# Kernel optimization log

Measured on AMD Instinct MI355X. Metric: run time of the kernel, lower is better.

Reference implementation:

```python
import jax, jax.numpy as jnp
import numpy as np

B = 2; D = 256; NH = 8; NL = 4; HD = D // NH
K = 2; P = K * K; NV = 4; DFF = 1024
SHAPES = ((128, 128), (64, 64), (32, 32), (16, 16))
LV = sum(h * w for h, w in SHAPES)
START = np.cumsum([0] + [h * w for h, w in SHAPES])[:-1].tolist()
EPS = 1e-5

# fixed 2x2 sampling kernel, matching _create_kernel_indices (even kernel branch)
_ind = np.linspace(-0.5, 0.5, K)
_ii, _jj = np.meshgrid(_ind, _ind, indexing='ij')
KERNEL = jnp.asarray(np.stack([_jj, _ii], -1).reshape(-1, 2) / K, jnp.float32)  # (P,2)


def _layer_norm(x, w, b):
    m = x.mean(-1, keepdims=True)
    v = ((x - m) ** 2).mean(-1, keepdims=True)
    return (x - m) * jax.lax.rsqrt(v + EPS) * w + b


def _box_attention(query, value, ref_windows, vpw, vpb, opw, opb, boxw, boxb, attw, attb):
    b, lq, _ = query.shape
    # value projection, split into heads: (b, NH, LV, HD)
    v = (value @ vpw.T + vpb).reshape(b, LV, NH, HD).transpose(0, 2, 1, 3)

    # attention weights: softmax over all (level, point) jointly per head
    aw = query @ attw.T + attb
    aw = jax.nn.softmax(aw.reshape(b, lq, NH, NL * P), -1).reshape(b, lq, NH, NL, P)

    # where to attend (with_rotation=False -> 4 offset variables, angle from ref)
    ob = (query @ boxw.T + boxb).reshape(b, lq, NH, NL, NV)
    rw = ref_windows[:, :, None, None, :]                    # (b,lq,1,1,7)
    ref_boxes = rw[..., jnp.array([0, 1, 3, 4])]
    angles = jnp.broadcast_to(rw[..., 6:7], (b, lq, NH, NL, 1))
    boxes = ref_boxes + ob / 8.0 * ref_boxes[..., jnp.array([2, 3, 2, 3])]
    center = boxes[..., None, :2]                            # (b,lq,NH,NL,1,2)
    size = boxes[..., None, 2:]
    c, s = jnp.cos(angles), jnp.sin(angles)
    rot = jnp.stack([c, -s, s, c], -1).reshape(b, lq, NH, NL, 1, 2, 2)
    g = KERNEL * jax.nn.relu(size)                           # (b,lq,NH,NL,P,2)
    grid = center + (g[..., None, :] * rot).sum(-1)          # (b,lq,NH,NL,P,2)

    # multi-level bilinear sampling (= grid_sample align_corners=False, zero pad)
    bidx = jnp.arange(b)[:, None, None, None]
    hidx = jnp.arange(NH)[None, None, :, None]
    out = jnp.zeros((b, lq, NH, HD), v.dtype)
    for lvl, (H, W) in enumerate(SHAPES):
        st = START[lvl]
        vl = v[:, :, st:st + H * W]                          # (b,NH,HW,HD)
        loc = grid[:, :, :, lvl]                             # (b,lq,NH,P,2)
        x = loc[..., 0] * W - 0.5
        y = loc[..., 1] * H - 0.5
        x0f = jnp.floor(x); y0f = jnp.floor(y)
        wx = x - x0f; wy = y - y0f
        x0 = x0f.astype(jnp.int32); y0 = y0f.astype(jnp.int32)
        acc = jnp.zeros((b, lq, NH, P, HD), v.dtype)
        corners = ((0, 0, (1 - wx) * (1 - wy)), (1, 0, wx * (1 - wy)),
                   (0, 1, (1 - wx) * wy), (1, 1, wx * wy))
        for dx, dy, wgt in corners:
            xi = x0 + dx; yi = y0 + dy
            valid = (xi >= 0) & (xi < W) & (yi >= 0) & (yi < H)
            idx = jnp.clip(yi, 0, H - 1) * W + jnp.clip(xi, 0, W - 1)
            samp = vl[bidx, hidx, idx]                       # (b,lq,NH,P,HD)
            acc = acc + (wgt * valid)[..., None] * samp
        out = out + jnp.einsum('blhp,blhpd->blhd', aw[:, :, :, lvl], acc)
    return out.reshape(b, lq, D) @ opw.T + opb


def setup_inputs() -> dict:
    key = jax.random.key(0)
    ks = jax.random.split(key, 20)
    def nrm(k, shape, fan_in):
        return jax.random.normal(k, shape, jnp.float32) * (1.0 / np.sqrt(fan_in))
    rw = jax.random.uniform(ks[2], (B, LV, 7), jnp.float32)
    # keep window sizes (cols 3,4,5) modest, like real BEV reference windows
    rw = rw.at[..., 3:6].multiply(0.2)
    return {
        'src': jax.random.normal(ks[0], (B, LV, D), jnp.float32),
        'pos': jax.random.normal(ks[1], (B, LV, D), jnp.float32),
        'src_shape': jnp.asarray(SHAPES, jnp.int32),
        'src_start_idx': jnp.asarray(START, jnp.int32),
        'ref_windows': rw,
        'vpw': nrm(ks[3], (D, D), D), 'vpb': jnp.zeros((D,), jnp.float32),
        'opw': nrm(ks[4], (D, D), D), 'opb': jnp.zeros((D,), jnp.float32),
        'boxw': nrm(ks[5], (NL * NH * NV, D), D) * 0.1,
        'boxb': jax.random.normal(ks[6], (NL * NH * NV,), jnp.float32) * 0.1,
        'attw': nrm(ks[7], (NH * NL * P, D), D),
        'attb': jnp.zeros((NH * NL * P,), jnp.float32),
        'lin1_w': nrm(ks[8], (DFF, D), D), 'lin1_b': jnp.zeros((DFF,), jnp.float32),
        'lin2_w': nrm(ks[9], (D, DFF), DFF), 'lin2_b': jnp.zeros((D,), jnp.float32),
        'ln1_w': jnp.ones((D,), jnp.float32), 'ln1_b': jnp.zeros((D,), jnp.float32),
        'ln2_w': jnp.ones((D,), jnp.float32), 'ln2_b': jnp.zeros((D,), jnp.float32),
    }


def reference(src, pos, src_shape, src_start_idx, ref_windows,
              vpw, vpb, opw, opb, boxw, boxb, attw, attb,
              lin1_w, lin1_b, lin2_w, lin2_b, ln1_w, ln1_b, ln2_w, ln2_b):
    # level shapes/starts are static (SHAPES/START constants); src_shape /
    # src_start_idx are accepted for signature fidelity.
    src2 = _box_attention(src + pos, src, ref_windows,
                          vpw, vpb, opw, opb, boxw, boxb, attw, attb)
    src = _layer_norm(src + src2, ln1_w, ln1_b)
    ffn = jax.nn.relu(src @ lin1_w.T + lin1_b) @ lin2_w.T + lin2_b
    return _layer_norm(src + ffn, ln2_w, ln2_b)
```

## Files before the change

### kernel.cpp

```cpp
#include <hip/hip_runtime.h>
#include <stdint.h>

typedef unsigned short u16;
typedef __attribute__((ext_vector_type(8))) short short8;
typedef __attribute__((ext_vector_type(4))) float f32x4;

#define D_    256
#define NH_   8
#define HD_   32
#define LV_   21760
#define DFF_  1024
#define EPS_  1e-5f
#define MH_   21760
#define MT_   43520

__device__ __forceinline__ float bf2f(u16 u) {
    union { uint32_t i; float f; } x; x.i = ((uint32_t)u) << 16; return x.f;
}
__device__ __forceinline__ u16 f2bf(float f) {
    union { float f; uint32_t i; } x; x.f = f;
    uint32_t r = x.i + 0x7FFFu + ((x.i >> 16) & 1u);
    return (u16)(r >> 16);
}
__device__ __forceinline__ uint32_t pk2(float a, float b) {
    return (uint32_t)f2bf(a) | ((uint32_t)f2bf(b) << 16);
}
__device__ __forceinline__ void cv8(u16* dst, float4 a, float4 b) {
    uint4 r;
    r.x = pk2(a.x, a.y); r.y = pk2(a.z, a.w);
    r.z = pk2(b.x, b.y); r.w = pk2(b.z, b.w);
    *(uint4*)dst = r;
}
__device__ __forceinline__ void cv8add(u16* dst, float4 a, float4 a2, float4 b, float4 b2) {
    uint4 r;
    r.x = pk2(a.x + a2.x, a.y + a2.y); r.y = pk2(a.z + a2.z, a.w + a2.w);
    r.z = pk2(b.x + b2.x, b.y + b2.y); r.w = pk2(b.z + b2.z, b.w + b2.w);
    *(uint4*)dst = r;
}

__global__ __launch_bounds__(256) void k_cvt(const float* __restrict__ in,
                                             u16* __restrict__ out, int n4) {
    int i = blockIdx.x * 256 + threadIdx.x;
    if (i < n4) {
        float4 v = ((const float4*)in)[i];
        uint2 r; r.x = pk2(v.x, v.y); r.y = pk2(v.z, v.w);
        *(uint2*)(out + (size_t)i * 4) = r;
    }
}

__global__ __launch_bounds__(256) void k_vprojm(
        const float* __restrict__ src, const float* __restrict__ vpw,
        const float* __restrict__ vpb, u16* __restrict__ vout) {
    __shared__ u16 As[2][64 * 32];
    __shared__ u16 Bs[2][64 * 32];
    const int t = threadIdx.x;
    const int l = t & 63, w = t >> 6;
    const int m0 = blockIdx.x * 64, n0 = blockIdx.y * 64;
    const int sr = t >> 2, sc = t & 3;
    const int wslot = sr * 32 + ((sc ^ ((sr >> 1) & 3)) << 3);
    const float* gA = src + (size_t)(m0 + sr) * 256 + sc * 8;
    const float* gB = vpw + (size_t)(n0 + sr) * 256 + sc * 8;
    const int fr = l & 15, fg = l >> 4;
    const int wm = w >> 1, wn = w & 1;

    f32x4 acc[2][2];
    #pragma unroll
    for (int mi = 0; mi < 2; ++mi)
        #pragma unroll
        for (int ni = 0; ni < 2; ++ni)
            acc[mi][ni] = (f32x4){0.f, 0.f, 0.f, 0.f};

    cv8(&As[0][wslot], *(const float4*)gA, *(const float4*)(gA + 4));
    cv8(&Bs[0][wslot], *(const float4*)gB, *(const float4*)(gB + 4));
    __syncthreads();

    for (int kt = 0; kt < 8; ++kt) {
        const int cur = kt & 1;
        float4 na0, na1, nb0, nb1;
        if (kt < 7) {
            na0 = *(const float4*)(gA + (kt + 1) * 32);
            na1 = *(const float4*)(gA + (kt + 1) * 32 + 4);
            nb0 = *(const float4*)(gB + (kt + 1) * 32);
            nb1 = *(const float4*)(gB + (kt + 1) * 32 + 4);
        }
        short8 af[2], bfr[2];
        #pragma unroll
        for (int mi = 0; mi < 2; ++mi) {
            const int r = wm * 32 + mi * 16 + fr;
            af[mi] = *(const short8*)&As[cur][r * 32 + ((fg ^ ((r >> 1) & 3)) << 3)];
        }
        #pragma unroll
        for (int ni = 0; ni < 2; ++ni) {
            const int r = wn * 32 + ni * 16 + fr;
            bfr[ni] = *(const short8*)&Bs[cur][r * 32 + ((fg ^ ((r >> 1) & 3)) << 3)];
        }
        #pragma unroll
        for (int mi = 0; mi < 2; ++mi)
            #pragma unroll
            for (int ni = 0; ni < 2; ++ni)
                acc[mi][ni] = __builtin_amdgcn_mfma_f32_16x16x32_bf16(af[mi], bfr[ni], acc[mi][ni], 0, 0, 0);
        if (kt < 7) {
            cv8(&As[cur ^ 1][wslot], na0, na1);
            cv8(&Bs[cur ^ 1][wslot], nb0, nb1);
            __syncthreads();
        }
    }
    const int b = m0 / LV_;
    #pragma unroll
    for (int ni = 0; ni < 2; ++ni) {
        const int n = n0 + wn * 32 + ni * 16 + fr;
        const float bv = vpb[n];
        const int h = n >> 5, hd = n & 31;
        #pragma unroll
        for (int mi = 0; mi < 2; ++mi) {
            #pragma unroll
            for (int q = 0; q < 4; ++q) {
                const int m = m0 + wm * 32 + mi * 16 + fg * 4 + q;
                const int lrow = m - b * LV_;
                vout[((size_t)(b * NH_ + h) * LV_ + lrow) * HD_ + hd] = f2bf(acc[mi][ni][q] + bv);
            }
        }
    }
}

__global__ __launch_bounds__(256) void k_logits(
        const float* __restrict__ src, const float* __restrict__ pos,
        const float* __restrict__ attw, const float* __restrict__ attb,
        const float* __restrict__ boxw, const float* __restrict__ boxb,
        float* __restrict__ logits) {
    __shared__ u16 As[2][64 * 32];
    __shared__ u16 Bs[2][64 * 32];
    const int t = threadIdx.x;
    const int l = t & 63, w = t >> 6;
    const int m0 = blockIdx.x * 64;
    const int n0g = blockIdx.y * 64;
    const float* Bsrc = (n0g < 128) ? (attw + (size_t)n0g * 256) : (boxw + (size_t)(n0g - 128) * 256);
    const float* bsrc = (n0g < 128) ? (attb + n0g) : (boxb + (n0g - 128));
    const int sr = t >> 2, sc = t & 3;
    const int wslot = sr * 32 + ((sc ^ ((sr >> 1) & 3)) << 3);
    const float* gAs = src + (size_t)(m0 + sr) * 256 + sc * 8;
    const float* gAp = pos + (size_t)(m0 + sr) * 256 + sc * 8;
    const float* gB  = Bsrc + (size_t)sr * 256 + sc * 8;
    const int fr = l & 15, fg = l >> 4;
    const int wm = w >> 1, wn = w & 1;

    f32x4 acc[2][2];
    #pragma unroll
    for (int mi = 0; mi < 2; ++mi)
        #pragma unroll
        for (int ni = 0; ni < 2; ++ni)
            acc[mi][ni] = (f32x4){0.f, 0.f, 0.f, 0.f};

    cv8add(&As[0][wslot], *(const float4*)gAs, *(const float4*)gAp,
                          *(const float4*)(gAs + 4), *(const float4*)(gAp + 4));
    cv8(&Bs[0][wslot], *(const float4*)gB, *(const float4*)(gB + 4));
    __syncthreads();

    for (int kt = 0; kt < 8; ++kt) {
        const int cur = kt & 1;
        float4 ns0, ns1, np0, np1, nb0, nb1;
        if (kt < 7) {
            ns0 = *(const float4*)(gAs + (kt + 1) * 32);
            ns1 = *(const float4*)(gAs + (kt + 1) * 32 + 4);
            np0 = *(const float4*)(gAp + (kt + 1) * 32);
            np1 = *(const float4*)(gAp + (kt + 1) * 32 + 4);
            nb0 = *(const float4*)(gB + (kt + 1) * 32);
            nb1 = *(const float4*)(gB + (kt + 1) * 32 + 4);
        }
        short8 af[2], bfr[2];
        #pragma unroll
        for (int mi = 0; mi < 2; ++mi) {
            const int r = wm * 32 + mi * 16 + fr;
            af[mi] = *(const short8*)&As[cur][r * 32 + ((fg ^ ((r >> 1) & 3)) << 3)];
        }
        #pragma unroll
        for (int ni = 0; ni < 2; ++ni) {
            const int r = wn * 32 + ni * 16 + fr;
            bfr[ni] = *(const short8*)&Bs[cur][r * 32 + ((fg ^ ((r >> 1) & 3)) << 3)];
        }
        #pragma unroll
        for (int mi = 0; mi < 2; ++mi)
            #pragma unroll
            for (int ni = 0; ni < 2; ++ni)
                acc[mi][ni] = __builtin_amdgcn_mfma_f32_16x16x32_bf16(af[mi], bfr[ni], acc[mi][ni], 0, 0, 0);
        if (kt < 7) {
            cv8add(&As[cur ^ 1][wslot], ns0, np0, ns1, np1);
            cv8(&Bs[cur ^ 1][wslot], nb0, nb1);
            __syncthreads();
        }
    }
    #pragma unroll
    for (int ni = 0; ni < 2; ++ni) {
        const int nl_ = wn * 32 + ni * 16 + fr;
        const float bv = bsrc[nl_];
        #pragma unroll
        for (int mi = 0; mi < 2; ++mi) {
            #pragma unroll
            for (int q = 0; q < 4; ++q) {
                const int m = m0 + wm * 32 + mi * 16 + fg * 4 + q;
                logits[(size_t)m * 256 + n0g + nl_] = acc[mi][ni][q] + bv;
            }
        }
    }
}

__global__ __launch_bounds__(256) void k_sample(
        const float* __restrict__ logits, const float* __restrict__ refw,
        const u16* __restrict__ vws, u16* __restrict__ smp) {
    __shared__ float AWL[8][128];
    __shared__ float OBL[8][128];
    __shared__ float CW[128][4];
    __shared__ int   CIDX[128][4];
    __shared__ float RW[8][8];
    const int t = threadIdx.x;
    const int bid = blockIdx.x;
    const int sb = (bid & 7) * (gridDim.x >> 3) + (bid >> 3);
    const long gr0 = (long)sb * 8;
    const int b = (int)(gr0 / LV_);
    {
        const float4* lp = (const float4*)(logits + gr0 * 256);
        #pragma unroll
        for (int i = 0; i < 2; ++i) {
            int ii = t + i * 256;
            float4 v = lp[ii];
            int r = ii >> 6, c4 = (ii & 63) << 2;
            float* dst = (c4 < 128) ? &AWL[r][c4] : &OBL[r][c4 - 128];
            dst[0] = v.x; dst[1] = v.y; dst[2] = v.z; dst[3] = v.w;
        }
        if (t < 56) {
            int r2 = t / 7, k = t % 7;
            RW[r2][k] = refw[(gr0 + r2) * 7 + k];
        }
    }
    __syncthreads();
    if (t < 64) {
        const int r = t >> 3, h = t & 7;
        float* a = &AWL[r][h * 16];
        float m = a[0];
        #pragma unroll
        for (int k = 1; k < 16; ++k) m = fmaxf(m, a[k]);
        float s = 0.f;
        float e[16];
        #pragma unroll
        for (int k = 0; k < 16; ++k) { e[k] = __expf(a[k] - m); s += e[k]; }
        const float inv = 1.f / s;
        #pragma unroll
        for (int k = 0; k < 16; ++k) a[k] = e[k] * inv;
    }
    for (int r = 0; r < 8; ++r) {
        __syncthreads();
        if (t < 128) {
            const int h = t >> 4, nl = (t >> 2) & 3, p = t & 3;
            const float rw0 = RW[r][0], rw1 = RW[r][1], rw3 = RW[r][3], rw4 = RW[r][4], ang = RW[r][6];
            const int obb = h * 16 + nl * 4;
            const float ob0 = OBL[r][obb + 0];
            const float ob1 = OBL[r][obb + 1];
            const float ob2 = OBL[r][obb + 2];
            const float ob3 = OBL[r][obb + 3];
            const float cx = rw0 + ob0 * 0.125f * rw3;
            const float cy = rw1 + ob1 * 0.125f * rw4;
            const float bw = fmaxf(rw3 + ob2 * 0.125f * rw3, 0.f);
            const float bh = fmaxf(rw4 + ob3 * 0.125f * rw4, 0.f);
            const float kx = (p & 1) ? 0.25f : -0.25f;
            const float ky = (p >> 1) ? 0.25f : -0.25f;
            float sth, cth;
            __sincosf(ang, &sth, &cth);
            const float g0 = kx * bw, g1 = ky * bh;
            const float gx = cx + g0 * cth - g1 * sth;
            const float gy = cy + g0 * sth + g1 * cth;
            const int Wl = 128 >> nl;
            const int st = (65536 - (65536 >> (2 * nl))) / 3;
            const float x = gx * Wl - 0.5f, y = gy * Wl - 0.5f;
            const float xf = floorf(x), yf = floorf(y);
            const float wx = x - xf, wy = y - yf;
            const int x0 = (int)xf, y0 = (int)yf;
            const float awv = AWL[r][t];
            #pragma unroll
            for (int c4 = 0; c4 < 4; ++c4) {
                const int dx = c4 & 1, dy = c4 >> 1;
                const int xi = x0 + dx, yi = y0 + dy;
                const float wgt = (dx ? wx : 1.f - wx) * (dy ? wy : 1.f - wy);
                const bool valid = (xi >= 0) && (xi < Wl) && (yi >= 0) && (yi < Wl);
                const int xc = xi < 0 ? 0 : (xi > Wl - 1 ? Wl - 1 : xi);
                const int yc = yi < 0 ? 0 : (yi > Wl - 1 ? Wl - 1 : yi);
                CW[t][c4] = valid ? wgt * awv : 0.f;
                CIDX[t][c4] = st + yc * Wl + xc;
            }
        }
        __syncthreads();
        {
            const int h = t >> 5, hd = t & 31;
            const size_t vbase = ((size_t)(b * NH_ + h) * LV_) * HD_ + hd;
            float acc = 0.f;
            #pragma unroll 4
            for (int k = 0; k < 16; ++k) {
                const int u = h * 16 + k;
                #pragma unroll
                for (int c4 = 0; c4 < 4; ++c4) {
                    const float w = CW[u][c4];
                    const int idx = CIDX[u][c4];
                    acc += w * bf2f(vws[vbase + (size_t)idx * HD_]);
                }
            }
            smp[(size_t)(gr0 + r) * 256 + t] = f2bf(acc);
        }
    }
}

__global__ __launch_bounds__(256) void k_oproj(
        const u16* __restrict__ A,
        const float* __restrict__ opw,
        const float* __restrict__ opb,
        const float* __restrict__ src,
        const float* __restrict__ lnw, const float* __restrict__ lnb,
        u16* __restrict__ out) {
    __shared__ char smem[36864];
    u16* As = (u16*)smem;
    u16* Bs = (u16*)(smem + 4096);
    float* Y = (float*)smem;
    const int t = threadIdx.x;
    const int l = t & 63, w = t >> 6;
    const int m0 = blockIdx.x * 32;
    const int sAr = t >> 2, sc = t & 3;
    const int aslot = sAr * 32 + ((sc ^ ((sAr >> 1) & 3)) << 3);
    const u16* gA = A + (size_t)(m0 + sAr) * 256 + sc * 8;
    const float* gB[4];
    int bslot[4];
    #pragma unroll
    for (int i = 0; i < 4; ++i) {
        const int r = (t >> 2) + i * 64;
        gB[i] = opw + (size_t)r * 256 + sc * 8;
        bslot[i] = r * 32 + ((sc ^ ((r >> 1) & 3)) << 3);
    }
    const int fr = l & 15, fg = l >> 4;

    f32x4 acc[2][4];
    #pragma unroll
    for (int mi = 0; mi < 2; ++mi)
        #pragma unroll
        for (int ni = 0; ni < 4; ++ni)
            acc[mi][ni] = (f32x4){0.f, 0.f, 0.f, 0.f};

    if (t < 128) *(uint4*)&As[aslot] = *(const uint4*)gA;
    #pragma unroll
    for (int i = 0; i < 4; ++i)
        cv8(&Bs[bslot[i]], *(const float4*)gB[i], *(const float4*)(gB[i] + 4));
    __syncthreads();

    for (int kt = 0; kt < 8; ++kt) {
        const int cur = kt & 1;
        uint4 na; float4 nb[4][2];
        if (kt < 7) {
            if (t < 128) na = *(const uint4*)(gA + (kt + 1) * 32);
            #pragma unroll
            for (int i = 0; i < 4; ++i) {
                nb[i][0] = *(const float4*)(gB[i] + (kt + 1) * 32);
                nb[i][1] = *(const float4*)(gB[i] + (kt + 1) * 32 + 4);
            }
        }
        short8 af[2], bfr[4];
        #pragma unroll
        for (int mi = 0; mi < 2; ++mi) {
            const int r = mi * 16 + fr;
            af[mi] = *(const short8*)&As[cur * 1024 + r * 32 + ((fg ^ ((r >> 1) & 3)) << 3)];
        }
        #pragma unroll
        for (int ni = 0; ni < 4; ++ni) {
            const int r = w * 64 + ni * 16 + fr;
            bfr[ni] = *(const short8*)&Bs[cur * 8192 + r * 32 + ((fg ^ ((r >> 1) & 3)) << 3)];
        }
        #pragma unroll
        for (int mi = 0; mi < 2; ++mi)
            #pragma unroll
            for (int ni = 0; ni < 4; ++ni)
                acc[mi][ni] = __builtin_amdgcn_mfma_f32_16x16x32_bf16(af[mi], bfr[ni], acc[mi][ni], 0, 0, 0);
        if (kt < 7) {
            if (t < 128) *(uint4*)&As[(cur ^ 1) * 1024 + aslot] = na;
            #pragma unroll
            for (int i = 0; i < 4; ++i)
                cv8(&Bs[(cur ^ 1) * 8192 + bslot[i]], nb[i][0], nb[i][1]);
            __syncthreads();
        }
    }
    __syncthreads();
    #pragma unroll
    for (int ni = 0; ni < 4; ++ni) {
        const int n = w * 64 + ni * 16 + fr;
        const float bv = opb[n];
        #pragma unroll
        for (int mi = 0; mi < 2; ++mi) {
            #pragma unroll
            for (int q = 0; q < 4; ++q) {
                const int ml = mi * 16 + fg * 4 + q;
                Y[ml * 256 + n] = acc[mi][ni][q] + bv + src[(size_t)(m0 + ml) * 256 + n];
            }
        }
    }
    __syncthreads();
    for (int rr = 0; rr < 8; ++rr) {
        const int m = w * 8 + rr;
        const float v0 = Y[m * 256 + l];
        const float v1 = Y[m * 256 + 64 + l];
        const float v2 = Y[m * 256 + 128 + l];
        const float v3 = Y[m * 256 + 192 + l];
        float s1 = v0 + v1 + v2 + v3;
        float s2 = v0 * v0 + v1 * v1 + v2 * v2 + v3 * v3;
        #pragma unroll
        for (int off = 32; off; off >>= 1) {
            s1 += __shfl_xor(s1, off);
            s2 += __shfl_xor(s2, off);
        }
        const float mean = s1 * (1.f / 256.f);
        const float var = s2 * (1.f / 256.f) - mean * mean;
        const float rs = rsqrtf(var + EPS_);
        const size_t ob = (size_t)(m0 + m) * 256;
        out[ob + l]       = f2bf((v0 - mean) * rs * lnw[l]       + lnb[l]);
        out[ob + 64 + l]  = f2bf((v1 - mean) * rs * lnw[64 + l]  + lnb[64 + l]);
        out[ob + 128 + l] = f2bf((v2 - mean) * rs * lnw[128 + l] + lnb[128 + l]);
        out[ob + 192 + l] = f2bf((v3 - mean) * rs * lnw[192 + l] + lnb[192 + l]);
    }
}

__global__ __launch_bounds__(256) void k_gemm1(
        const u16* __restrict__ A, const u16* __restrict__ Bw,
        const float* __restrict__ bias, u16* __restrict__ H) {
    __shared__ u16 As[2][64 * 32];
    __shared__ u16 Bs[2][64 * 32];
    const int t = threadIdx.x;
    const int l = t & 63, w = t >> 6;
    const int m0 = blockIdx.x * 64, n0 = blockIdx.y * 64;
    const int sr = t >> 2, sc = t & 3;
    const int wslot = sr * 32 + ((sc ^ ((sr >> 1) & 3)) << 3);
    const u16* gA = A + (size_t)(m0 + sr) * 256 + sc * 8;
    const u16* gB = Bw + (size_t)(n0 + sr) * 256 + sc * 8;
    const int fr = l & 15, fg = l >> 4;
    const int wm = w >> 1, wn = w & 1;

    f32x4 acc[2][2];
    #pragma unroll
    for (int mi = 0; mi < 2; ++mi)
        #pragma unroll
        for (int ni = 0; ni < 2; ++ni)
            acc[mi][ni] = (f32x4){0.f, 0.f, 0.f, 0.f};

    *(uint4*)&As[0][wslot] = *(const uint4*)(gA);
    *(uint4*)&Bs[0][wslot] = *(const uint4*)(gB);
    __syncthreads();

    for (int kt = 0; kt < 8; ++kt) {
        const int cur = kt & 1;
        uint4 na, nb;
        if (kt < 7) {
            na = *(const uint4*)(gA + (kt + 1) * 32);
            nb = *(const uint4*)(gB + (kt + 1) * 32);
        }
        short8 af[2], bfr[2];
        #pragma unroll
        for (int mi = 0; mi < 2; ++mi) {
            const int r = wm * 32 + mi * 16 + fr;
            af[mi] = *(const short8*)&As[cur][r * 32 + ((fg ^ ((r >> 1) & 3)) << 3)];
        }
        #pragma unroll
        for (int ni = 0; ni < 2; ++ni) {
            const int r = wn * 32 + ni * 16 + fr;
            bfr[ni] = *(const short8*)&Bs[cur][r * 32 + ((fg ^ ((r >> 1) & 3)) << 3)];
        }
        #pragma unroll
        for (int mi = 0; mi < 2; ++mi)
            #pragma unroll
            for (int ni = 0; ni < 2; ++ni)
                acc[mi][ni] = __builtin_amdgcn_mfma_f32_16x16x32_bf16(af[mi], bfr[ni], acc[mi][ni], 0, 0, 0);
        if (kt < 7) {
            *(uint4*)&As[cur ^ 1][wslot] = na;
            *(uint4*)&Bs[cur ^ 1][wslot] = nb;
            __syncthreads();
        }
    }
    #pragma unroll
    for (int ni = 0; ni < 2; ++ni) {
        const int n = n0 + wn * 32 + ni * 16 + fr;
        const float bv = bias[n];
        #pragma unroll
        for (int mi = 0; mi < 2; ++mi) {
            #pragma unroll
            for (int q = 0; q < 4; ++q) {
                const int m = m0 + wm * 32 + mi * 16 + fg * 4 + q;
                const float v = acc[mi][ni][q] + bv;
                H[(size_t)m * 1024 + n] = f2bf(fmaxf(v, 0.f));
            }
        }
    }
}

__global__ __launch_bounds__(256) void k_gemm2(
        const u16* __restrict__ A, const u16* __restrict__ Bw,
        const float* __restrict__ bias, const u16* __restrict__ resid,
        const float* __restrict__ lnw, const float* __restrict__ lnb,
        float* __restrict__ out) {
    __shared__ char smem[36864];
    u16* As = (u16*)smem;
    u16* Bs = (u16*)(smem + 4096);
    float* Y = (float*)smem;
    const int t = threadIdx.x;
    const int l = t & 63, w = t >> 6;
    const int m0 = blockIdx.x * 32;
    const int sAr = t >> 2, sc = t & 3;
    const int aslot = sAr * 32 + ((sc ^ ((sAr >> 1) & 3)) << 3);
    const u16* gA = A + (size_t)(m0 + sAr) * 1024 + sc * 8;
    const u16* gB[4];
    int bslot[4];
    #pragma unroll
    for (int i = 0; i < 4; ++i) {
        const int r = (t >> 2) + i * 64;
        gB[i] = Bw + (size_t)r * 1024 + sc * 8;
        bslot[i] = r * 32 + ((sc ^ ((r >> 1) & 3)) << 3);
    }
    const int fr = l & 15, fg = l >> 4;

    f32x4 acc[2][4];
    #pragma unroll
    for (int mi = 0; mi < 2; ++mi)
        #pragma unroll
        for (int ni = 0; ni < 4; ++ni)
            acc[mi][ni] = (f32x4){0.f, 0.f, 0.f, 0.f};

    if (t < 128) *(uint4*)&As[aslot] = *(const uint4*)(gA);
    #pragma unroll
    for (int i = 0; i < 4; ++i) *(uint4*)&Bs[bslot[i]] = *(const uint4*)(gB[i]);
    __syncthreads();

    for (int kt = 0; kt < 32; ++kt) {
        const int cur = kt & 1;
        uint4 na, nb[4];
        if (kt < 31) {
            if (t < 128) na = *(const uint4*)(gA + (kt + 1) * 32);
            #pragma unroll
            for (int i = 0; i < 4; ++i) nb[i] = *(const uint4*)(gB[i] + (kt + 1) * 32);
        }
        short8 af[2], bfr[4];
        #pragma unroll
        for (int mi = 0; mi < 2; ++mi) {
            const int r = mi * 16 + fr;
            af[mi] = *(const short8*)&As[cur * 1024 + r * 32 + ((fg ^ ((r >> 1) & 3)) << 3)];
        }
        #pragma unroll
        for (int ni = 0; ni < 4; ++ni) {
            const int r = w * 64 + ni * 16 + fr;
            bfr[ni] = *(const short8*)&Bs[cur * 8192 + r * 32 + ((fg ^ ((r >> 1) & 3)) << 3)];
        }
        #pragma unroll
        for (int mi = 0; mi < 2; ++mi)
            #pragma unroll
            for (int ni = 0; ni < 4; ++ni)
                acc[mi][ni] = __builtin_amdgcn_mfma_f32_16x16x32_bf16(af[mi], bfr[ni], acc[mi][ni], 0, 0, 0);
        if (kt < 31) {
            if (t < 128) *(uint4*)&As[(cur ^ 1) * 1024 + aslot] = na;
            #pragma unroll
            for (int i = 0; i < 4; ++i) *(uint4*)&Bs[(cur ^ 1) * 8192 + bslot[i]] = nb[i];
            __syncthreads();
        }
    }
    __syncthreads();
    #pragma unroll
    for (int ni = 0; ni < 4; ++ni) {
        const int n = w * 64 + ni * 16 + fr;
        const float bv = bias[n];
        #pragma unroll
        for (int mi = 0; mi < 2; ++mi) {
            #pragma unroll
            for (int q = 0; q < 4; ++q) {
                const int ml = mi * 16 + fg * 4 + q;
                Y[ml * 256 + n] = acc[mi][ni][q] + bv + bf2f(resid[(size_t)(m0 + ml) * 256 + n]);
            }
        }
    }
    __syncthreads();
    for (int rr = 0; rr < 8; ++rr) {
        const int m = w * 8 + rr;
        const float v0 = Y[m * 256 + l];
        const float v1 = Y[m * 256 + 64 + l];
        const float v2 = Y[m * 256 + 128 + l];
        const float v3 = Y[m * 256 + 192 + l];
        float s1 = v0 + v1 + v2 + v3;
        float s2 = v0 * v0 + v1 * v1 + v2 * v2 + v3 * v3;
        #pragma unroll
        for (int off = 32; off; off >>= 1) {
            s1 += __shfl_xor(s1, off);
            s2 += __shfl_xor(s2, off);
        }
        const float mean = s1 * (1.f / 256.f);
        const float var = s2 * (1.f / 256.f) - mean * mean;
        const float rs = rsqrtf(var + EPS_);
        const size_t ob = (size_t)(m0 + m) * 256;
        out[ob + l]        = (v0 - mean) * rs * lnw[l]        + lnb[l];
        out[ob + 64 + l]   = (v1 - mean) * rs * lnw[64 + l]   + lnb[64 + l];
        out[ob + 128 + l]  = (v2 - mean) * rs * lnw[128 + l]  + lnb[128 + l];
        out[ob + 192 + l]  = (v3 - mean) * rs * lnw[192 + l]  + lnb[192 + l];
    }
}

extern "C" void kernel_launch(void* const* d_in, const int* in_sizes, int n_in,
                              void* d_out, int out_size, void* d_ws, size_t ws_size,
                              hipStream_t stream) {
    const float* src  = (const float*)d_in[0];
    const float* pos  = (const float*)d_in[1];
    const float* refw = (const float*)d_in[4];
    const float* vpw  = (const float*)d_in[5];
    const float* vpb  = (const float*)d_in[6];
    const float* opw  = (const float*)d_in[7];
    const float* opb  = (const float*)d_in[8];
    const float* boxw = (const float*)d_in[9];
    const float* boxb = (const float*)d_in[10];
    const float* attw = (const float*)d_in[11];
    const float* attb = (const float*)d_in[12];
    const float* l1w  = (const float*)d_in[13];
    const float* l1b  = (const float*)d_in[14];
    const float* l2w  = (const float*)d_in[15];
    const float* l2b  = (const float*)d_in[16];
    const float* ln1w = (const float*)d_in[17];
    const float* ln1b = (const float*)d_in[18];
    const float* ln2w = (const float*)d_in[19];
    const float* ln2b = (const float*)d_in[20];

    u16*   vws    = (u16*)d_ws;
    u16*   l1wb   = (u16*)d_ws;
    u16*   l2wb   = (u16*)((char*)d_ws + 524288);
    float* logits = (float*)((char*)d_ws + 22282240u);
    u16*   src1b  = (u16*)((char*)d_ws + 22282240u);
    u16*   Hbf    = (u16*)((char*)d_ws + 44564480u);
    u16*   smp    = (u16*)((char*)d_ws + 66846720u);

    hipLaunchKernelGGL(k_vprojm, dim3(680, 4), dim3(256), 0, stream, src, vpw, vpb, vws);
    hipLaunchKernelGGL(k_logits, dim3(680, 4), dim3(256), 0, stream,
                       src, pos, attw, attb, boxw, boxb, logits);
    hipLaunchKernelGGL(k_sample, dim3(5440), dim3(256), 0, stream, logits, refw, vws, smp);
    hipLaunchKernelGGL(k_cvt, dim3(256), dim3(256), 0, stream, l1w, l1wb, 65536);
    hipLaunchKernelGGL(k_cvt, dim3(256), dim3(256), 0, stream, l2w, l2wb, 65536);
    hipLaunchKernelGGL(k_oproj, dim3(1360), dim3(256), 0, stream,
                       smp, opw, opb, src, ln1w, ln1b, src1b);
    for (int h = 0; h < 2; ++h) {
        const u16* Ah = src1b + (size_t)h * MH_ * 256;
        float* outh   = (float*)d_out + (size_t)h * MH_ * 256;
        hipLaunchKernelGGL(k_gemm1, dim3(340, 16), dim3(256), 0, stream, Ah, l1wb, l1b, Hbf);
        hipLaunchKernelGGL(k_gemm2, dim3(680), dim3(256), 0, stream, Hbf, l2wb, l2b, Ah, ln2w, ln2b, outh);
    }
}
```

Measured before the change: 364.9 us.

## Vectorize box-attention gather over 4 channels and enlarge FFN gemm1 tiles

The sampling kernel now computes corner weights and indices for four query rows at once using all 256 threads. It packs weights and byte offsets together in one padded shared buffer. Each thread then gathers four bf16 channels per load with 8-byte reads instead of one scalar bf16 per thread, which cuts the sync count and the number of gather instructions. Separately, gemm1 moves from 64x64 to 128x128 tiles with 4x4 MFMA fragments per wave, raising data reuse at the cost of more registers and fewer blocks.

```diff
diff --git a/kernel.cpp b/kernel.cpp
--- a/kernel.cpp
+++ b/kernel.cpp
@@ -24,6 +24,12 @@
 }
 __device__ __forceinline__ uint32_t pk2(float a, float b) {
     return (uint32_t)f2bf(a) | ((uint32_t)f2bf(b) << 16);
+}
+__device__ __forceinline__ float blo(uint32_t u) {
+    union { uint32_t i; float f; } x; x.i = u << 16; return x.f;
+}
+__device__ __forceinline__ float bhi(uint32_t u) {
+    union { uint32_t i; float f; } x; x.i = u & 0xffff0000u; return x.f;
 }
 __device__ __forceinline__ void cv8(u16* dst, float4 a, float4 b) {
     uint4 r;
@@ -209,8 +215,7 @@
         const u16* __restrict__ vws, u16* __restrict__ smp) {
     __shared__ float AWL[8][128];
     __shared__ float OBL[8][128];
-    __shared__ float CW[128][4];
-    __shared__ int   CIDX[128][4];
+    __shared__ __align__(16) uint2 CWI[128 * 18];
     __shared__ float RW[8][8];
     const int t = threadIdx.x;
     const int bid = blockIdx.x;
@@ -224,8 +229,8 @@
             int ii = t + i * 256;
             float4 v = lp[ii];
             int r = ii >> 6, c4 = (ii & 63) << 2;
-            float* dst = (c4 < 128) ? &AWL[r][c4] : &OBL[r][c4 - 128];
-            dst[0] = v.x; dst[1] = v.y; dst[2] = v.z; dst[3] = v.w;
+            if (c4 < 128) *(float4*)&AWL[r][c4] = v;
+            else          *(float4*)&OBL[r][c4 - 128] = v;
         }
         if (t < 56) {
             int r2 = t / 7, k = t % 7;
@@ -247,34 +252,46 @@
         #pragma unroll
         for (int k = 0; k < 16; ++k) a[k] = e[k] * inv;
     }
-    for (int r = 0; r < 8; ++r) {
-        __syncthreads();
-        if (t < 128) {
-            const int h = t >> 4, nl = (t >> 2) & 3, p = t & 3;
-            const float rw0 = RW[r][0], rw1 = RW[r][1], rw3 = RW[r][3], rw4 = RW[r][4], ang = RW[r][6];
-            const int obb = h * 16 + nl * 4;
-            const float ob0 = OBL[r][obb + 0];
-            const float ob1 = OBL[r][obb + 1];
-            const float ob2 = OBL[r][obb + 2];
-            const float ob3 = OBL[r][obb + 3];
+    __syncthreads();
+
+    const int e = t & 7;
+    const int g = t >> 3;
+    const int rloc_g = g & 3, hg = g >> 2;
+    const char* vbp = (const char*)vws +
+        (((size_t)(b * NH_ + hg) * LV_) * HD_ + e * 4) * 2;
+    const int cu = t & 127, rsel = t >> 7;
+    const int ch = cu >> 4, cnl = (cu >> 2) & 3, cp = cu & 3;
+
+    for (int wdw = 0; wdw < 2; ++wdw) {
+        #pragma unroll
+        for (int rr = 0; rr < 2; ++rr) {
+            const int rloc = rsel * 2 + rr;
+            const int row = wdw * 4 + rloc;
+            const float rw0 = RW[row][0], rw1 = RW[row][1], rw3 = RW[row][3], rw4 = RW[row][4], ang = RW[row][6];
+            const int obb = ch * 16 + cnl * 4;
+            const float ob0 = OBL[row][obb + 0];
+            const float ob1 = OBL[row][obb + 1];
+            const float ob2 = OBL[row][obb + 2];
+            const float ob3 = OBL[row][obb + 3];
             const float cx = rw0 + ob0 * 0.125f * rw3;
             const float cy = rw1 + ob1 * 0.125f * rw4;
             const float bw = fmaxf(rw3 + ob2 * 0.125f * rw3, 0.f);
             const float bh = fmaxf(rw4 + ob3 * 0.125f * rw4, 0.f);
-            const float kx = (p & 1) ? 0.25f : -0.25f;
-            const float ky = (p >> 1) ? 0.25f : -0.25f;
+            const float kx = (cp & 1) ? 0.25f : -0.25f;
+            const float ky = (cp >> 1) ? 0.25f : -0.25f;
             float sth, cth;
             __sincosf(ang, &sth, &cth);
             const float g0 = kx * bw, g1 = ky * bh;
             const float gx = cx + g0 * cth - g1 * sth;
             const float gy = cy + g0 * sth + g1 * cth;
-            const int Wl = 128 >> nl;
-            const int st = (65536 - (65536 >> (2 * nl))) / 3;
+            const int Wl = 128 >> cnl;
+            const int st = (65536 - (65536 >> (2 * cnl))) / 3;
             const float x = gx * Wl - 0.5f, y = gy * Wl - 0.5f;
             const float xf = floorf(x), yf = floorf(y);
             const float wx = x - xf, wy = y - yf;
             const int x0 = (int)xf, y0 = (int)yf;
-            const float awv = AWL[r][t];
+            const float awv = AWL[row][cu];
+            uint2 cw[4];
             #pragma unroll
             for (int c4 = 0; c4 < 4; ++c4) {
                 const int dx = c4 & 1, dy = c4 >> 1;
@@ -283,27 +300,38 @@
                 const bool valid = (xi >= 0) && (xi < Wl) && (yi >= 0) && (yi < Wl);
                 const int xc = xi < 0 ? 0 : (xi > Wl - 1 ? Wl - 1 : xi);
                 const int yc = yi < 0 ? 0 : (yi > Wl - 1 ? Wl - 1 : yi);
-                CW[t][c4] = valid ? wgt * awv : 0.f;
-                CIDX[t][c4] = st + yc * Wl + xc;
-            }
+                const float wv = valid ? wgt * awv : 0.f;
+                cw[c4].x = __float_as_uint(wv);
+                cw[c4].y = (uint32_t)(st + yc * Wl + xc) * 64u;
+            }
+            uint2* dst = &CWI[cu * 18 + rloc * 4];
+            *(uint4*)(dst)     = *(const uint4*)&cw[0];
+            *(uint4*)(dst + 2) = *(const uint4*)&cw[2];
         }
         __syncthreads();
         {
-            const int h = t >> 5, hd = t & 31;
-            const size_t vbase = ((size_t)(b * NH_ + h) * LV_) * HD_ + hd;
-            float acc = 0.f;
+            const int row = wdw * 4 + rloc_g;
+            float a0 = 0.f, a1 = 0.f, a2 = 0.f, a3 = 0.f;
             #pragma unroll 4
             for (int k = 0; k < 16; ++k) {
-                const int u = h * 16 + k;
+                const int ub = (hg * 16 + k) * 18 + rloc_g * 4;
                 #pragma unroll
-                for (int c4 = 0; c4 < 4; ++c4) {
-                    const float w = CW[u][c4];
-                    const int idx = CIDX[u][c4];
-                    acc += w * bf2f(vws[vbase + (size_t)idx * HD_]);
+                for (int cc = 0; cc < 2; ++cc) {
+                    const uint4 cw2 = *(const uint4*)&CWI[ub + cc * 2];
+                    const float w0 = __uint_as_float(cw2.x);
+                    const uint2 d0 = *(const uint2*)(vbp + cw2.y);
+                    const float w1 = __uint_as_float(cw2.z);
+                    const uint2 d1 = *(const uint2*)(vbp + cw2.w);
+                    a0 += w0 * blo(d0.x); a1 += w0 * bhi(d0.x);
+                    a2 += w0 * blo(d0.y); a3 += w0 * bhi(d0.y);
+                    a0 += w1 * blo(d1.x); a1 += w1 * bhi(d1.x);
+                    a2 += w1 * blo(d1.y); a3 += w1 * bhi(d1.y);
                 }
             }
-            smp[(size_t)(gr0 + r) * 256 + t] = f2bf(acc);
-        }
+            uint2 o; o.x = pk2(a0, a1); o.y = pk2(a2, a3);
+            *(uint2*)(smp + (size_t)(gr0 + row) * 256 + hg * 32 + e * 4) = o;
+        }
+        __syncthreads();
     }
 }
 
@@ -424,67 +452,74 @@
 __global__ __launch_bounds__(256) void k_gemm1(
         const u16* __restrict__ A, const u16* __restrict__ Bw,
         const float* __restrict__ bias, u16* __restrict__ H) {
-    __shared__ u16 As[2][64 * 32];
-    __shared__ u16 Bs[2][64 * 32];
+    __shared__ u16 As[2][128 * 32];
+    __shared__ u16 Bs[2][128 * 32];
     const int t = threadIdx.x;
     const int l = t & 63, w = t >> 6;
-    const int m0 = blockIdx.x * 64, n0 = blockIdx.y * 64;
-    const int sr = t >> 2, sc = t & 3;
-    const int wslot = sr * 32 + ((sc ^ ((sr >> 1) & 3)) << 3);
-    const u16* gA = A + (size_t)(m0 + sr) * 256 + sc * 8;
-    const u16* gB = Bw + (size_t)(n0 + sr) * 256 + sc * 8;
+    const int m0 = blockIdx.x * 128, n0 = blockIdx.y * 128;
+    const int sr = t >> 1, sc0 = (t & 1) * 2;
+    const int ws0 = sr * 32 + ((sc0 ^ ((sr >> 1) & 3)) << 3);
+    const int ws1 = sr * 32 + (((sc0 + 1) ^ ((sr >> 1) & 3)) << 3);
+    const u16* gA = A + (size_t)(m0 + sr) * 256 + sc0 * 8;
+    const u16* gB = Bw + (size_t)(n0 + sr) * 256 + sc0 * 8;
     const int fr = l & 15, fg = l >> 4;
     const int wm = w >> 1, wn = w & 1;
 
-    f32x4 acc[2][2];
-    #pragma unroll
-    for (int mi = 0; mi < 2; ++mi)
-        #pragma unroll
-        for (int ni = 0; ni < 2; ++ni)
+    f32x4 acc[4][4];
+    #pragma unroll
+    for (int mi = 0; mi < 4; ++mi)
+        #pragma unroll
+        for (int ni = 0; ni < 4; ++ni)
             acc[mi][ni] = (f32x4){0.f, 0.f, 0.f, 0.f};
 
-    *(uint4*)&As[0][wslot] = *(const uint4*)(gA);
-    *(uint4*)&Bs[0][wslot] = *(const uint4*)(gB);
+    *(uint4*)&As[0][ws0] = *(const uint4*)(gA);
+    *(uint4*)&As[0][ws1] = *(const uint4*)(gA + 8);
+    *(uint4*)&Bs[0][ws0] = *(const uint4*)(gB);
+    *(uint4*)&Bs[0][ws1] = *(const uint4*)(gB + 8);
     __syncthreads();
 
     for (int kt = 0; kt < 8; ++kt) {
         const int cur = kt & 1;
-        uint4 na, nb;
-        if (kt < 7) {
-            na = *(const uint4*)(gA + (kt + 1) * 32);
-            nb = *(const uint4*)(gB + (kt + 1) * 32);
-        }
-        short8 af[2], bfr[2];
-        #pragma unroll
-        for (int mi = 0; mi < 2; ++mi) {
-            const int r = wm * 32 + mi * 16 + fr;
+        uint4 na0, na1, nb0, nb1;
+        if (kt < 7) {
+            na0 = *(const uint4*)(gA + (kt + 1) * 32);
+            na1 = *(const uint4*)(gA + (kt + 1) * 32 + 8);
+            nb0 = *(const uint4*)(gB + (kt + 1) * 32);
+            nb1 = *(const uint4*)(gB + (kt + 1) * 32 + 8);
+        }
+        short8 af[4], bfr[4];
+        #pragma unroll
+        for (int mi = 0; mi < 4; ++mi) {
+            const int r = wm * 64 + mi * 16 + fr;
             af[mi] = *(const short8*)&As[cur][r * 32 + ((fg ^ ((r >> 1) & 3)) << 3)];
         }
         #pragma unroll
-        for (int ni = 0; ni < 2; ++ni) {
-            const int r = wn * 32 + ni * 16 + fr;
+        for (int ni = 0; ni < 4; ++ni) {
+            const int r = wn * 64 + ni * 16 + fr;
             bfr[ni] = *(const short8*)&Bs[cur][r * 32 + ((fg ^ ((r >> 1) & 3)) << 3)];
         }
         #pragma unroll
-        for (int mi = 0; mi < 2; ++mi)
-            #pragma unroll
-            for (int ni = 0; ni < 2; ++ni)
+        for (int mi = 0; mi < 4; ++mi)
+            #pragma unroll
+            for (int ni = 0; ni < 4; ++ni)
                 acc[mi][ni] = __builtin_amdgcn_mfma_f32_16x16x32_bf16(af[mi], bfr[ni], acc[mi][ni], 0, 0, 0);
         if (kt < 7) {
-            *(uint4*)&As[cur ^ 1][wslot] = na;
-            *(uint4*)&Bs[cur ^ 1][wslot] = nb;
+            *(uint4*)&As[cur ^ 1][ws0] = na0;
+            *(uint4*)&As[cur ^ 1][ws1] = na1;
+            *(uint4*)&Bs[cur ^ 1][ws0] = nb0;
+            *(uint4*)&Bs[cur ^ 1][ws1] = nb1;
             __syncthreads();
         }
     }
     #pragma unroll
-    for (int ni = 0; ni < 2; ++ni) {
-        const int n = n0 + wn * 32 + ni * 16 + fr;
+    for (int ni = 0; ni < 4; ++ni) {
+        const int n = n0 + wn * 64 + ni * 16 + fr;
         const float bv = bias[n];
         #pragma unroll
-        for (int mi = 0; mi < 2; ++mi) {
+        for (int mi = 0; mi < 4; ++mi) {
             #pragma unroll
             for (int q = 0; q < 4; ++q) {
-                const int m = m0 + wm * 32 + mi * 16 + fg * 4 + q;
+                const int m = m0 + wm * 64 + mi * 16 + fg * 4 + q;
                 const float v = acc[mi][ni][q] + bv;
                 H[(size_t)m * 1024 + n] = f2bf(fmaxf(v, 0.f));
             }
@@ -641,7 +676,7 @@
     for (int h = 0; h < 2; ++h) {
         const u16* Ah = src1b + (size_t)h * MH_ * 256;
         float* outh   = (float*)d_out + (size_t)h * MH_ * 256;
-        hipLaunchKernelGGL(k_gemm1, dim3(340, 16), dim3(256), 0, stream, Ah, l1wb, l1b, Hbf);
+        hipLaunchKernelGGL(k_gemm1, dim3(170, 8), dim3(256), 0, stream, Ah, l1wb, l1b, Hbf);
         hipLaunchKernelGGL(k_gemm2, dim3(680), dim3(256), 0, stream, Hbf, l2wb, l2b, Ah, ln2w, ln2b, outh);
     }
 }
```

Result: faster. 356.5 us (-2.3%).
